# Kernel tuning notes

Hardware: AMD Instinct MI355X
Metric: run time of the kernel (lower is better)

The kernel has to match this reference:

```python
import jax, jax.numpy as jnp
import numpy as np

N_NODES = 50000
N_EDGES = 800000
IN_DIM = 128
EMB = 128
EDGE_DIM = 16
N_LAYERS = 4
BATCH = 64


def setup_inputs() -> dict:
    key = jax.random.key(0)
    ks = jax.random.split(key, 12)
    x = jax.random.normal(ks[0], (N_NODES, IN_DIM), dtype=jnp.float32)
    edge_index = jax.random.randint(ks[1], (2, N_EDGES), 0, N_NODES, dtype=jnp.int64)
    edge_attr = jax.random.normal(ks[2], (N_EDGES, EDGE_DIM), dtype=jnp.float32)
    batch = jnp.sort(jax.random.randint(ks[3], (N_NODES,), 0, BATCH, dtype=jnp.int64))

    def glorot(k, shape):
        fan_in = shape[-2]
        return jax.random.normal(k, shape, dtype=jnp.float32) / jnp.sqrt(jnp.float32(fan_in))

    msg_in = 2 * EMB + EDGE_DIM  # [h_src, h_dst, edge_attr]
    upd_in = 2 * EMB             # [h, aggregated_messages]
    return {
        "x": x,
        "edge_index": edge_index,
        "edge_attr": edge_attr,
        "batch": batch,
        "W_in": glorot(ks[4], (IN_DIM, EMB)),
        "b_in": jnp.zeros((EMB,), jnp.float32),
        "W_msg": glorot(ks[5], (N_LAYERS, msg_in, EMB)),
        "b_msg": jnp.zeros((N_LAYERS, EMB), jnp.float32),
        "W_upd": glorot(ks[6], (N_LAYERS, upd_in, EMB)),
        "b_upd": jnp.zeros((N_LAYERS, EMB), jnp.float32),
        "W_pred": glorot(ks[7], (EMB, 1)),
        "b_pred": jnp.zeros((1,), jnp.float32),
    }


def reference(x, edge_index, edge_attr, batch,
              W_in, b_in, W_msg, b_msg, W_upd, b_upd, W_pred, b_pred):
    n_nodes = x.shape[0]
    src, dst = edge_index[0], edge_index[1]

    # lin_in
    h = x @ W_in + b_in  # [N, EMB]

    # stacked message-passing layers with residual adds
    for l in range(W_msg.shape[0]):  # small fixed layer loop
        # per-edge message: relu(Linear([h_src, h_dst, e]))
        m_in = jnp.concatenate([h[src], h[dst], edge_attr], axis=-1)  # [E, 2*EMB+ED]
        m = jax.nn.relu(m_in @ W_msg[l] + b_msg[l])                    # [E, EMB]
        # sum-aggregate messages at destination nodes
        agg = jax.ops.segment_sum(m, dst, num_segments=n_nodes)       # [N, EMB]
        # node update: relu(Linear([h, agg])); residual add (h = h + conv(h))
        u_in = jnp.concatenate([h, agg], axis=-1)                      # [N, 2*EMB]
        h = h + jax.nn.relu(u_in @ W_upd[l] + b_upd[l])

    # global mean pool over graphs in the batch
    counts = jax.ops.segment_sum(jnp.ones((n_nodes,), h.dtype), batch, num_segments=BATCH)
    h_graph = jax.ops.segment_sum(h, batch, num_segments=BATCH) / jnp.maximum(counts, 1.0)[:, None]

    # lin_pred + view(-1)
    out = h_graph @ W_pred + b_pred  # [BATCH, 1]
    return out.reshape(-1)
```

## Files before the change

### kernel.cpp

```cpp
#include <hip/hip_runtime.h>


#define THREADS 256

typedef __attribute__((ext_vector_type(8))) short short8v;
typedef __attribute__((ext_vector_type(4))) float f32x4;
typedef __attribute__((ext_vector_type(2))) float f32x2;

__device__ inline unsigned short f2bf(float f)
{
    unsigned int u = __float_as_uint(f);
    return (unsigned short)((u + 0x7FFFu + ((u >> 16) & 1u)) >> 16);
}

__device__ inline unsigned int cvt_pk_bf16(float lo, float hi)
{
    unsigned int r;
    asm("v_cvt_pk_bf16_f32 %0, %1, %2" : "=v"(r) : "v"(lo), "v"(hi));
    return r;
}

__global__ __launch_bounds__(THREADS)
void wconv_all(const float* __restrict__ W_in, const float* __restrict__ W_msg,
               const float* __restrict__ W_upd, unsigned short* __restrict__ wbf)
{
    int b = blockIdx.x;
    int job, kb;
    if (b < 576) { job = b >> 6; kb = b & 63; }
    else         { int r = b - 576; job = 9 + (r >> 7); kb = r & 127; }

    const float* src;
    unsigned short* dst;
    int K;
    if (job == 0)      { src = W_in;                                  dst = wbf;                               K = 128; }
    else if (job <= 4) { int l = job - 1; src = W_msg + (size_t)l * 272 * 128;             dst = wbf + 16384 + l * 32768;           K = 128; }
    else if (job <= 8) { int l = job - 5; src = W_msg + (size_t)l * 272 * 128 + 128 * 128; dst = wbf + 16384 + l * 32768 + 16384;   K = 128; }
    else               { int l = job - 9; src = W_upd + (size_t)l * 256 * 128;             dst = wbf + 147456 + l * 32768;          K = 256; }

    int i = kb * 256 + threadIdx.x;
    int k = i >> 7, n = i & 127;
    dst[n * K + k] = f2bf(src[i]);
}

__global__ __launch_bounds__(THREADS)
void f32_to_bf16(const float* __restrict__ in, unsigned short* __restrict__ out, int n4)
{
    int i = blockIdx.x * blockDim.x + threadIdx.x;
    int stride = gridDim.x * blockDim.x;
    for (; i < n4; i += stride) {
        float4 v = reinterpret_cast<const float4*>(in)[i];
        unsigned int lo = f2bf(v.x) | ((unsigned int)f2bf(v.y) << 16);
        unsigned int hi = f2bf(v.z) | ((unsigned int)f2bf(v.w) << 16);
        reinterpret_cast<uint2*>(out)[i] = make_uint2(lo, hi);
    }
}

template<int K, int CPW, bool FUSED2, bool RELU, bool RESID>
__global__ __launch_bounds__(THREADS)
void gemm_regW(const unsigned short* __restrict__ X1, const unsigned short* __restrict__ X2,
               const unsigned short* __restrict__ Wt, const float* __restrict__ bias,
               const unsigned short* __restrict__ resid,
               unsigned short* __restrict__ CbfA, unsigned short* __restrict__ CbfB,
               int M, int nTiles)
{
    constexpr int KS  = K / 32;
    constexpr int NC  = CPW * 64;
    constexpr int LST = NC + 4;
    __shared__ float Cls[32 * LST];

    const int t = threadIdx.x;
    const int w = t >> 6;
    const int l = t & 63;
    const int r  = l & 15;
    const int kb = l >> 4;
    const int wc = w * (CPW * 16);

    short8v b[CPW][KS];
#pragma unroll
    for (int c = 0; c < CPW; c++)
#pragma unroll
        for (int ks = 0; ks < KS; ks++)
            b[c][ks] = *reinterpret_cast<const short8v*>(
                Wt + (size_t)(wc + c * 16 + r) * K + ks * 32 + kb * 8);

    const int rrow = t >> 3;
    const int cb   = (t & 7) * (NC / 8);

    for (int tile = blockIdx.x; tile < nTiles; tile += gridDim.x) {
        const int mBase = tile * 32;
        const int row0 = min(mBase + r,      M - 1);
        const int row1 = min(mBase + 16 + r, M - 1);

        f32x4 acc[2][CPW];
#pragma unroll
        for (int mi = 0; mi < 2; mi++)
#pragma unroll
            for (int c = 0; c < CPW; c++) acc[mi][c] = (f32x4){0.f, 0.f, 0.f, 0.f};

#pragma unroll
        for (int ks = 0; ks < KS; ks++) {
            const unsigned short* Xs = X1;
            int ko = ks * 32;
            if (K == 256 && ko >= 128) { Xs = X2; ko -= 128; }
            const short8v a0 = *reinterpret_cast<const short8v*>(Xs + (size_t)row0 * 128 + ko + kb * 8);
            const short8v a1 = *reinterpret_cast<const short8v*>(Xs + (size_t)row1 * 128 + ko + kb * 8);
#pragma unroll
            for (int c = 0; c < CPW; c++) {
                acc[0][c] = __builtin_amdgcn_mfma_f32_16x16x32_bf16(a0, b[c][ks], acc[0][c], 0, 0, 0);
                acc[1][c] = __builtin_amdgcn_mfma_f32_16x16x32_bf16(a1, b[c][ks], acc[1][c], 0, 0, 0);
            }
        }

#pragma unroll
        for (int mi = 0; mi < 2; mi++)
#pragma unroll
            for (int c = 0; c < CPW; c++) {
                const int gc = wc + c * 16 + r;
#pragma unroll
                for (int j = 0; j < 4; j++)
                    Cls[(mi * 16 + kb * 4 + j) * LST + gc] = acc[mi][c][j];
            }
        __syncthreads();

        const int gr = mBase + rrow;
        if (gr < M) {
#pragma unroll
            for (int q = 0; q < NC / 64; q += 1) {
                f32x4 v0 = *reinterpret_cast<const f32x4*>(&Cls[rrow * LST + cb + q * 8]);
                f32x4 v1 = *reinterpret_cast<const f32x4*>(&Cls[rrow * LST + cb + q * 8 + 4]);
                const int col = cb + q * 8;

                if (FUSED2) {
                    if (col >= 128) {
                        v0 += *reinterpret_cast<const f32x4*>(bias + col - 128);
                        v1 += *reinterpret_cast<const f32x4*>(bias + col - 128 + 4);
                    }
                } else if (bias) {
                    v0 += *reinterpret_cast<const f32x4*>(bias + col);
                    v1 += *reinterpret_cast<const f32x4*>(bias + col + 4);
                }
                if (RELU) {
#pragma unroll
                    for (int i = 0; i < 4; i++) { v0[i] = fmaxf(v0[i], 0.f); v1[i] = fmaxf(v1[i], 0.f); }
                }
                if (RESID) {
                    uint4 rv = *reinterpret_cast<const uint4*>(resid + (size_t)gr * 128 + col);
                    v0[0] += __uint_as_float(rv.x << 16);
                    v0[1] += __uint_as_float(rv.x & 0xFFFF0000u);
                    v0[2] += __uint_as_float(rv.y << 16);
                    v0[3] += __uint_as_float(rv.y & 0xFFFF0000u);
                    v1[0] += __uint_as_float(rv.z << 16);
                    v1[1] += __uint_as_float(rv.z & 0xFFFF0000u);
                    v1[2] += __uint_as_float(rv.w << 16);
                    v1[3] += __uint_as_float(rv.w & 0xFFFF0000u);
                }
                uint4 pk;
                pk.x = cvt_pk_bf16(v0[0], v0[1]);
                pk.y = cvt_pk_bf16(v0[2], v0[3]);
                pk.z = cvt_pk_bf16(v1[0], v1[1]);
                pk.w = cvt_pk_bf16(v1[2], v1[3]);
                if (FUSED2) {
                    if (col < 128)
                        *reinterpret_cast<uint4*>(CbfA + (size_t)gr * 128 + col) = pk;
                    else
                        *reinterpret_cast<uint4*>(CbfB + (size_t)gr * 128 + col - 128) = pk;
                } else {
                    *reinterpret_cast<uint4*>(CbfA + (size_t)gr * 128 + col) = pk;
                }
            }
        }
        __syncthreads();
    }
}

__global__ __launch_bounds__(THREADS)
void zero_i32(int* __restrict__ p, int n)
{
    int i = blockIdx.x * blockDim.x + threadIdx.x;
    int stride = gridDim.x * blockDim.x;
    for (; i < n; i += stride) p[i] = 0;
}


__global__ __launch_bounds__(THREADS)
void csr_hist(const int* __restrict__ edst, int* __restrict__ deg, int nE)
{
    int i = blockIdx.x * blockDim.x + threadIdx.x;
    int stride = gridDim.x * blockDim.x;
    for (; i < nE; i += stride) atomicAdd(&deg[edst[i]], 1);
}

__global__ __launch_bounds__(THREADS)
void scan_stage1(const int* __restrict__ deg, int* __restrict__ incl,
                 int* __restrict__ psum, int n)
{
    __shared__ int buf[THREADS];
    const int t = threadIdx.x;
    const int base = blockIdx.x * 1024 + t * 4;

    int v0 = (base + 0 < n) ? deg[base + 0] : 0;
    int v1 = (base + 1 < n) ? deg[base + 1] : 0;
    int v2 = (base + 2 < n) ? deg[base + 2] : 0;
    int v3 = (base + 3 < n) ? deg[base + 3] : 0;
    const int s = v0 + v1 + v2 + v3;

    buf[t] = s;
    __syncthreads();
#pragma unroll
    for (int off = 1; off < THREADS; off <<= 1) {
        int x = (t >= off) ? buf[t - off] : 0;
        __syncthreads();
        buf[t] += x;
        __syncthreads();
    }
    const int excl = buf[t] - s;

    if (base + 0 < n) incl[base + 0] = excl + v0;
    if (base + 1 < n) incl[base + 1] = excl + v0 + v1;
    if (base + 2 < n) incl[base + 2] = excl + v0 + v1 + v2;
    if (base + 3 < n) incl[base + 3] = excl + s;
    if (t == THREADS - 1) psum[blockIdx.x] = buf[THREADS - 1];
}

__global__ __launch_bounds__(THREADS)
void scan_stage2(int* __restrict__ psum, int nb)
{
    __shared__ int buf[THREADS];
    const int t = threadIdx.x;
    int v = (t < nb) ? psum[t] : 0;
    buf[t] = v;
    __syncthreads();
#pragma unroll
    for (int off = 1; off < THREADS; off <<= 1) {
        int x = (t >= off) ? buf[t - off] : 0;
        __syncthreads();
        buf[t] += x;
        __syncthreads();
    }
    if (t < nb) psum[t] = buf[t] - v;
}

__global__ __launch_bounds__(THREADS)
void scan_stage3(const int* __restrict__ incl, const int* __restrict__ deg,
                 const int* __restrict__ psum, int* __restrict__ rowptr,
                 int* __restrict__ wp, int n, int nE)
{
    int i = blockIdx.x * blockDim.x + threadIdx.x;
    int stride = gridDim.x * blockDim.x;
    for (; i < n; i += stride) {
        int ex = incl[i] - deg[i] + psum[i >> 10];
        rowptr[i] = ex;
        wp[i]     = ex;
    }
    if (blockIdx.x == 0 && threadIdx.x == 0) rowptr[n] = nE;
}

__global__ __launch_bounds__(THREADS)
void csr_scatter(const int* __restrict__ esrc, const int* __restrict__ edst,
                 int* __restrict__ wp, int2* __restrict__ colord, int nE)
{
    int i = blockIdx.x * blockDim.x + threadIdx.x;
    int stride = gridDim.x * blockDim.x;
    for (; i < nE; i += stride) {
        int d = edst[i];
        int pos = atomicAdd(&wp[d], 1);
        colord[pos] = make_int2(esrc[i], i);
    }
}

__global__ __launch_bounds__(THREADS)
void eattr_gather(const float* __restrict__ eattr, const int2* __restrict__ colord,
                  float* __restrict__ eattrp, int nQ)
{
    int i = blockIdx.x * blockDim.x + threadIdx.x;
    int stride = gridDim.x * blockDim.x;
    for (; i < nQ; i += stride) {
        const int p = i >> 2, j = i & 3;
        const int orig = colord[p].y;
        reinterpret_cast<float4*>(eattrp)[(size_t)p * 4 + j] =
            reinterpret_cast<const float4*>(eattr)[(size_t)orig * 4 + j];
    }
}

__global__ __launch_bounds__(THREADS)
void edge_agg(const unsigned short* __restrict__ A, const unsigned short* __restrict__ Bb,
              const float* __restrict__ eattrp, const int2* __restrict__ colord,
              const int* __restrict__ rowptr, const float* __restrict__ Wm3,
              unsigned short* __restrict__ agg, int nN)
{
    __shared__ float W3s[16 * 128];
    const int t = threadIdx.x;

    *reinterpret_cast<float4*>(&W3s[t * 4])        = *reinterpret_cast<const float4*>(Wm3 + t * 4);
    *reinterpret_cast<float4*>(&W3s[1024 + t * 4]) = *reinterpret_cast<const float4*>(Wm3 + 1024 + t * 4);
    __syncthreads();

    const int lane = t & 63;
    const int wid  = __builtin_amdgcn_readfirstlane(t >> 6);
    const int d    = blockIdx.x * 4 + wid;
    if (d >= nN) return;

    f32x2 w[16];
#pragma unroll
    for (int k = 0; k < 16; k++)
        w[k] = *reinterpret_cast<const f32x2*>(&W3s[k * 128 + lane * 2]);

    const unsigned int bu = *reinterpret_cast<const unsigned int*>(Bb + (size_t)d * 128 + lane * 2);
    const f32x2 bv = (f32x2){__uint_as_float(bu << 16), __uint_as_float(bu & 0xFFFF0000u)};
    const f32x2 zero = (f32x2){0.f, 0.f};
    f32x2 acc = zero;

    const int beg = rowptr[d], end = rowptr[d + 1];
    int e = beg;
    for (; e + 4 <= end; e += 4) {
        const int2 c0 = colord[e + 0];
        const int2 c1 = colord[e + 1];
        const int2 c2 = colord[e + 2];
        const int2 c3 = colord[e + 3];
        const unsigned int au0 = *reinterpret_cast<const unsigned int*>(A + (size_t)c0.x * 128 + lane * 2);
        const unsigned int au1 = *reinterpret_cast<const unsigned int*>(A + (size_t)c1.x * 128 + lane * 2);
        const unsigned int au2 = *reinterpret_cast<const unsigned int*>(A + (size_t)c2.x * 128 + lane * 2);
        const unsigned int au3 = *reinterpret_cast<const unsigned int*>(A + (size_t)c3.x * 128 + lane * 2);
        const f32x4* pe = reinterpret_cast<const f32x4*>(eattrp + (size_t)e * 16);
        const f32x4 e00 = pe[0],  e01 = pe[1],  e02 = pe[2],  e03 = pe[3];
        const f32x4 e10 = pe[4],  e11 = pe[5],  e12 = pe[6],  e13 = pe[7];
        const f32x4 e20 = pe[8],  e21 = pe[9],  e22 = pe[10], e23 = pe[11];
        const f32x4 e30 = pe[12], e31 = pe[13], e32 = pe[14], e33 = pe[15];

        __builtin_amdgcn_sched_group_barrier(0x020, 24, 0);
        __builtin_amdgcn_sched_group_barrier(0x002, 160, 0);

        f32x2 v0 = (f32x2){__uint_as_float(au0 << 16), __uint_as_float(au0 & 0xFFFF0000u)} + bv;
        f32x2 v1 = (f32x2){__uint_as_float(au1 << 16), __uint_as_float(au1 & 0xFFFF0000u)} + bv;
        f32x2 v2 = (f32x2){__uint_as_float(au2 << 16), __uint_as_float(au2 & 0xFFFF0000u)} + bv;
        f32x2 v3 = (f32x2){__uint_as_float(au3 << 16), __uint_as_float(au3 & 0xFFFF0000u)} + bv;

        const float ek0[16] = {e00[0], e00[1], e00[2], e00[3], e01[0], e01[1], e01[2], e01[3],
                               e02[0], e02[1], e02[2], e02[3], e03[0], e03[1], e03[2], e03[3]};
        const float ek1[16] = {e10[0], e10[1], e10[2], e10[3], e11[0], e11[1], e11[2], e11[3],
                               e12[0], e12[1], e12[2], e12[3], e13[0], e13[1], e13[2], e13[3]};
        const float ek2[16] = {e20[0], e20[1], e20[2], e20[3], e21[0], e21[1], e21[2], e21[3],
                               e22[0], e22[1], e22[2], e22[3], e23[0], e23[1], e23[2], e23[3]};
        const float ek3[16] = {e30[0], e30[1], e30[2], e30[3], e31[0], e31[1], e31[2], e31[3],
                               e32[0], e32[1], e32[2], e32[3], e33[0], e33[1], e33[2], e33[3]};
#pragma unroll
        for (int k = 0; k < 16; k++) {
            v0 = __builtin_elementwise_fma((f32x2){ek0[k], ek0[k]}, w[k], v0);
            v1 = __builtin_elementwise_fma((f32x2){ek1[k], ek1[k]}, w[k], v1);
            v2 = __builtin_elementwise_fma((f32x2){ek2[k], ek2[k]}, w[k], v2);
            v3 = __builtin_elementwise_fma((f32x2){ek3[k], ek3[k]}, w[k], v3);
        }
        acc += __builtin_elementwise_max(v0, zero) + __builtin_elementwise_max(v1, zero)
             + __builtin_elementwise_max(v2, zero) + __builtin_elementwise_max(v3, zero);
    }
    for (; e < end; e++) {
        const int s = colord[e].x;
        const unsigned int au = *reinterpret_cast<const unsigned int*>(A + (size_t)s * 128 + lane * 2);
        f32x2 v = (f32x2){__uint_as_float(au << 16), __uint_as_float(au & 0xFFFF0000u)} + bv;
        const f32x4* ep = reinterpret_cast<const f32x4*>(eattrp + (size_t)e * 16);
        const f32x4 f0 = ep[0], f1 = ep[1], f2 = ep[2], f3 = ep[3];
        const float ek[16] = {f0[0], f0[1], f0[2], f0[3], f1[0], f1[1], f1[2], f1[3],
                              f2[0], f2[1], f2[2], f2[3], f3[0], f3[1], f3[2], f3[3]};
#pragma unroll
        for (int k = 0; k < 16; k++)
            v = __builtin_elementwise_fma((f32x2){ek[k], ek[k]}, w[k], v);
        acc += __builtin_elementwise_max(v, zero);
    }
    *reinterpret_cast<unsigned int*>(agg + (size_t)d * 128 + lane * 2) = cvt_pk_bf16(acc[0], acc[1]);
}


__global__ __launch_bounds__(THREADS)
void pool_partial(const unsigned short* __restrict__ hbf, const int* __restrict__ batch,
                  float* __restrict__ hgsum, int n)
{
    const int t    = threadIdx.x;
    const int c    = t & 127;
    const int half = t >> 7;
    const int beg  = blockIdx.x * 256;
    const int end  = min(beg + 256, n);
    if (beg >= n) return;

    int   cur = -1;
    float acc = 0.f;
    for (int r = beg + half; r < end; r += 2) {
        int g = batch[r];
        if (g != cur) {
            if (cur >= 0) atomicAdd(&hgsum[(size_t)cur * 128 + c], acc);
            cur = g; acc = 0.f;
        }
        acc += __uint_as_float((unsigned int)hbf[(size_t)r * 128 + c] << 16);
    }
    if (cur >= 0) atomicAdd(&hgsum[(size_t)cur * 128 + c], acc);
}

__global__ __launch_bounds__(THREADS)
void pool_final(const float* __restrict__ hgsum, const int* __restrict__ batch,
                const float* __restrict__ Wp, const float* __restrict__ bp,
                float* __restrict__ out, int n)
{
    __shared__ float red[128];
    const int g = blockIdx.x;
    const int t = threadIdx.x;
    if (t >= 128) return;

    int lo, hi;
    {
        int a = 0, b = n;
        while (a < b) { int m = (a + b) >> 1; if (batch[m] < g) a = m + 1; else b = m; }
        lo = a;
        b = n;
        while (a < b) { int m = (a + b) >> 1; if (batch[m] < g + 1) a = m + 1; else b = m; }
        hi = a;
    }
    const int cnt = hi - lo;

    float v = hgsum[(size_t)g * 128 + t] / (float)max(cnt, 1);
    red[t] = v * Wp[t];
    __syncthreads();
    for (int off = 64; off > 0; off >>= 1) {
        if (t < off) red[t] += red[t + off];
        __syncthreads();
    }
    if (t == 0) out[g] = red[0] + bp[0];
}

extern "C" void kernel_launch(void* const* d_in, const int* in_sizes, int n_in,
                              void* d_out, int out_size, void* d_ws, size_t ws_size,
                              hipStream_t stream)
{
    const float* x      = (const float*)d_in[0];
    const int*   ei     = (const int*)  d_in[1];
    const float* eattr  = (const float*)d_in[2];
    const int*   batch  = (const int*)  d_in[3];
    const float* W_in   = (const float*)d_in[4];
    const float* b_in   = (const float*)d_in[5];
    const float* W_msg  = (const float*)d_in[6];
    const float* b_msg  = (const float*)d_in[7];
    const float* W_upd  = (const float*)d_in[8];
    const float* b_upd  = (const float*)d_in[9];
    const float* W_pred = (const float*)d_in[10];
    const float* b_pred = (const float*)d_in[11];
    float* out = (float*)d_out;

    const int nN = in_sizes[0] / 128;
    const int nE = in_sizes[1] / 2;
    const int* esrc = ei;
    const int* edst = ei + nE;

    float* hgsum  = (float*)d_ws;
    float* eattrp = hgsum + 8192;
    unsigned short* xbf    = (unsigned short*)(eattrp + (size_t)nE * 16);
    unsigned short* h_bf   = xbf    + (size_t)nN * 128;
    unsigned short* A_bf   = h_bf   + (size_t)nN * 128;
    unsigned short* Bb_bf  = A_bf   + (size_t)nN * 128;
    unsigned short* agg_bf = Bb_bf  + (size_t)nN * 128;
    unsigned short* wbf    = agg_bf + (size_t)nN * 128;
    unsigned short* wt_in  = wbf;
    unsigned short* wt_msg = wbf + 16384;
    unsigned short* wt_up  = wbf + 147456;
    int2*  colord = (int2*)(wbf + 278528);
    int*   rowptr = (int*)(colord + nE);
    int*   wp     = rowptr + (nN + 1);
    int*   deg    = wp     + nN;
    int*   incl   = deg    + nN;
    int*   psum   = incl   + nN;

    dim3 blk(THREADS);
    const int nTiles = (nN + 31) / 32;
    const int gGemm  = 512;
    const int nChunks = (nN + 1023) / 1024;

    wconv_all<<<1088, blk, 0, stream>>>(W_in, W_msg, W_upd, wbf);
    f32_to_bf16<<<1024, blk, 0, stream>>>(x, xbf, nN * 128 / 4);

    zero_i32<<<64, blk, 0, stream>>>(deg, nN);
    csr_hist<<<256, blk, 0, stream>>>(edst, deg, nE);
    scan_stage1<<<nChunks, blk, 0, stream>>>(deg, incl, psum, nN);
    scan_stage2<<<1, blk, 0, stream>>>(psum, nChunks);
    scan_stage3<<<64, blk, 0, stream>>>(incl, deg, psum, rowptr, wp, nN, nE);
    csr_scatter<<<2048, blk, 0, stream>>>(esrc, edst, wp, colord, nE);
    eattr_gather<<<2048, blk, 0, stream>>>(eattr, colord, eattrp, nE * 4);

    gemm_regW<128, 2, false, false, false><<<gGemm, blk, 0, stream>>>(
        xbf, nullptr, wt_in, b_in, nullptr, h_bf, nullptr, nN, nTiles);

    for (int l = 0; l < 4; l++) {
        const float* Wm3 = W_msg + (size_t)l * 272 * 128 + 256 * 128;
        const float* bm  = b_msg + l * 128;
        const float* bu  = b_upd + l * 128;

        gemm_regW<128, 4, true, false, false><<<gGemm, blk, 0, stream>>>(
            h_bf, nullptr, wt_msg + l * 32768, bm, nullptr, A_bf, Bb_bf, nN, nTiles);

        edge_agg<<<(nN + 3) / 4, blk, 0, stream>>>(A_bf, Bb_bf, eattrp, colord, rowptr, Wm3, agg_bf, nN);

        gemm_regW<256, 2, false, true, true><<<gGemm, blk, 0, stream>>>(
            h_bf, agg_bf, wt_up + l * 32768, bu, h_bf, h_bf, nullptr, nN, nTiles);
    }

    zero_i32<<<16, blk, 0, stream>>>((int*)hgsum, 64 * 128);
    pool_partial<<<(nN + 255) / 256, blk, 0, stream>>>(h_bf, batch, hgsum, nN);
    pool_final<<<64, blk, 0, stream>>>(hgsum, batch, W_pred, b_pred, out, nN);
}
```

Before: 666.0 us.

## Fuse edge-attribute permutation into CSR scatter, shrink column index, double GEMM grid

The separate eattr_gather kernel is folded into csr_scatter: each edge reads its attributes contiguously and writes them to the CSR position it obtains from the atomic. The column array drops the original edge id and becomes a plain int array, which halves the index traffic read by edge_agg. The manual scheduling group barriers in edge_agg are removed, and the GEMM grid size goes from 512 to 1024 blocks. The scatter writes 64-byte rows to random positions rather than doing coalesced writes, and the GEMM grid change alters per-block work.

Measured after the change: 581.9 us. 12.6% less time.

```diff
diff --git a/kernel.cpp b/kernel.cpp
--- a/kernel.cpp
+++ b/kernel.cpp
@@ -257,34 +257,25 @@
 
 __global__ __launch_bounds__(THREADS)
 void csr_scatter(const int* __restrict__ esrc, const int* __restrict__ edst,
-                 int* __restrict__ wp, int2* __restrict__ colord, int nE)
+                 const float* __restrict__ eattr, int* __restrict__ wp,
+                 int* __restrict__ col, float* __restrict__ eattrp, int nE)
 {
     int i = blockIdx.x * blockDim.x + threadIdx.x;
     int stride = gridDim.x * blockDim.x;
     for (; i < nE; i += stride) {
         int d = edst[i];
+        const float4* src4 = reinterpret_cast<const float4*>(eattr + (size_t)i * 16);
+        float4 r0 = src4[0], r1 = src4[1], r2 = src4[2], r3 = src4[3];
         int pos = atomicAdd(&wp[d], 1);
-        colord[pos] = make_int2(esrc[i], i);
-    }
-}
-
-__global__ __launch_bounds__(THREADS)
-void eattr_gather(const float* __restrict__ eattr, const int2* __restrict__ colord,
-                  float* __restrict__ eattrp, int nQ)
-{
-    int i = blockIdx.x * blockDim.x + threadIdx.x;
-    int stride = gridDim.x * blockDim.x;
-    for (; i < nQ; i += stride) {
-        const int p = i >> 2, j = i & 3;
-        const int orig = colord[p].y;
-        reinterpret_cast<float4*>(eattrp)[(size_t)p * 4 + j] =
-            reinterpret_cast<const float4*>(eattr)[(size_t)orig * 4 + j];
+        col[pos] = esrc[i];
+        float4* dst4 = reinterpret_cast<float4*>(eattrp + (size_t)pos * 16);
+        dst4[0] = r0; dst4[1] = r1; dst4[2] = r2; dst4[3] = r3;
     }
 }
 
 __global__ __launch_bounds__(THREADS)
 void edge_agg(const unsigned short* __restrict__ A, const unsigned short* __restrict__ Bb,
-              const float* __restrict__ eattrp, const int2* __restrict__ colord,
+              const float* __restrict__ eattrp, const int* __restrict__ col,
               const int* __restrict__ rowptr, const float* __restrict__ Wm3,
               unsigned short* __restrict__ agg, int nN)
 {
@@ -313,22 +304,19 @@
     const int beg = rowptr[d], end = rowptr[d + 1];
     int e = beg;
     for (; e + 4 <= end; e += 4) {
-        const int2 c0 = colord[e + 0];
-        const int2 c1 = colord[e + 1];
-        const int2 c2 = colord[e + 2];
-        const int2 c3 = colord[e + 3];
-        const unsigned int au0 = *reinterpret_cast<const unsigned int*>(A + (size_t)c0.x * 128 + lane * 2);
-        const unsigned int au1 = *reinterpret_cast<const unsigned int*>(A + (size_t)c1.x * 128 + lane * 2);
-        const unsigned int au2 = *reinterpret_cast<const unsigned int*>(A + (size_t)c2.x * 128 + lane * 2);
-        const unsigned int au3 = *reinterpret_cast<const unsigned int*>(A + (size_t)c3.x * 128 + lane * 2);
+        const int s0 = col[e + 0];
+        const int s1 = col[e + 1];
+        const int s2 = col[e + 2];
+        const int s3 = col[e + 3];
+        const unsigned int au0 = *reinterpret_cast<const unsigned int*>(A + (size_t)s0 * 128 + lane * 2);
+        const unsigned int au1 = *reinterpret_cast<const unsigned int*>(A + (size_t)s1 * 128 + lane * 2);
+        const unsigned int au2 = *reinterpret_cast<const unsigned int*>(A + (size_t)s2 * 128 + lane * 2);
+        const unsigned int au3 = *reinterpret_cast<const unsigned int*>(A + (size_t)s3 * 128 + lane * 2);
         const f32x4* pe = reinterpret_cast<const f32x4*>(eattrp + (size_t)e * 16);
         const f32x4 e00 = pe[0],  e01 = pe[1],  e02 = pe[2],  e03 = pe[3];
         const f32x4 e10 = pe[4],  e11 = pe[5],  e12 = pe[6],  e13 = pe[7];
         const f32x4 e20 = pe[8],  e21 = pe[9],  e22 = pe[10], e23 = pe[11];
         const f32x4 e30 = pe[12], e31 = pe[13], e32 = pe[14], e33 = pe[15];
-
-        __builtin_amdgcn_sched_group_barrier(0x020, 24, 0);
-        __builtin_amdgcn_sched_group_barrier(0x002, 160, 0);
 
         f32x2 v0 = (f32x2){__uint_as_float(au0 << 16), __uint_as_float(au0 & 0xFFFF0000u)} + bv;
         f32x2 v1 = (f32x2){__uint_as_float(au1 << 16), __uint_as_float(au1 & 0xFFFF0000u)} + bv;
@@ -354,7 +342,7 @@
              + __builtin_elementwise_max(v2, zero) + __builtin_elementwise_max(v3, zero);
     }
     for (; e < end; e++) {
-        const int s = colord[e].x;
+        const int s = col[e];
         const unsigned int au = *reinterpret_cast<const unsigned int*>(A + (size_t)s * 128 + lane * 2);
         f32x2 v = (f32x2){__uint_as_float(au << 16), __uint_as_float(au & 0xFFFF0000u)} + bv;
         const f32x4* ep = reinterpret_cast<const f32x4*>(eattrp + (size_t)e * 16);
@@ -459,8 +447,8 @@
     unsigned short* wt_in  = wbf;
     unsigned short* wt_msg = wbf + 16384;
     unsigned short* wt_up  = wbf + 147456;
-    int2*  colord = (int2*)(wbf + 278528);
-    int*   rowptr = (int*)(colord + nE);
+    int*   col    = (int*)(wbf + 278528);
+    int*   rowptr = col    + nE;
     int*   wp     = rowptr + (nN + 1);
     int*   deg    = wp     + nN;
     int*   incl   = deg    + nN;
@@ -468,7 +456,7 @@
 
     dim3 blk(THREADS);
     const int nTiles = (nN + 31) / 32;
-    const int gGemm  = 512;
+    const int gGemm  = 1024;
     const int nChunks = (nN + 1023) / 1024;
 
     wconv_all<<<1088, blk, 0, stream>>>(W_in, W_msg, W_upd, wbf);
@@ -479,8 +467,7 @@
     scan_stage1<<<nChunks, blk, 0, stream>>>(deg, incl, psum, nN);
     scan_stage2<<<1, blk, 0, stream>>>(psum, nChunks);
     scan_stage3<<<64, blk, 0, stream>>>(incl, deg, psum, rowptr, wp, nN, nE);
-    csr_scatter<<<2048, blk, 0, stream>>>(esrc, edst, wp, colord, nE);
-    eattr_gather<<<2048, blk, 0, stream>>>(eattr, colord, eattrp, nE * 4);
+    csr_scatter<<<2048, blk, 0, stream>>>(esrc, edst, eattr, wp, col, eattrp, nE);
 
     gemm_regW<128, 2, false, false, false><<<gGemm, blk, 0, stream>>>(
         xbf, nullptr, wt_in, b_in, nullptr, h_bf, nullptr, nN, nTiles);
@@ -493,7 +480,7 @@
         gemm_regW<128, 4, true, false, false><<<gGemm, blk, 0, stream>>>(
             h_bf, nullptr, wt_msg + l * 32768, bm, nullptr, A_bf, Bb_bf, nN, nTiles);
 
-        edge_agg<<<(nN + 3) / 4, blk, 0, stream>>>(A_bf, Bb_bf, eattrp, colord, rowptr, Wm3, agg_bf, nN);
+        edge_agg<<<(nN + 3) / 4, blk, 0, stream>>>(A_bf, Bb_bf, eattrp, col, rowptr, Wm3, agg_bf, nN);
 
         gemm_regW<256, 2, false, true, true><<<gGemm, blk, 0, stream>>>(
             h_bf, agg_bf, wt_up + l * 32768, bu, h_bf, h_bf, nullptr, nN, nTiles);
```
